# Optimization experiments

Hardware: AMD Instinct MI355X
Metric: run time of the kernel (lower is better)

The kernel has to match this reference:

```python
import jax, jax.numpy as jnp
import numpy as np

B, C, D, E, ES, TOPK = 8, 4096, 1024, 16, 256, 4096

def setup_inputs() -> dict:
    key = jax.random.key(0)
    k1, k2, k3, k4 = jax.random.split(key, 4)
    x = jax.random.normal(k1, (B, C, D), dtype=jnp.float32)
    gate = jax.random.normal(k2, (C, E), dtype=jnp.float32) / np.sqrt(D)
    lin1_weight = jax.random.normal(k3, (D, E, ES), dtype=jnp.float32) / np.sqrt(D)
    lin2_weight = jax.random.normal(k4, (E, ES, D), dtype=jnp.float32) / np.sqrt(ES)
    return {"x": x, "gate": gate, "lin1_weight": lin1_weight, "lin2_weight": lin2_weight, "topk": TOPK}

def reference(x, gate, lin1_weight, lin2_weight, topk):
    b, c, d = x.shape
    e = gate.shape[1]
    n_tokens = b * c
    # faithful to original einsum: sum x over dmodel, elementwise-mult by gate[c, e]
    gate_out = jnp.einsum('bcd,ce->bce', x, gate)            # [b, c, e]
    gate_out = jnp.transpose(gate_out, (2, 0, 1)).reshape(e, n_tokens)
    gate_out = jax.nn.softmax(gate_out, axis=1)              # softmax over tokens per expert
    topk_values, topk_indices = jax.lax.top_k(gate_out, topk)  # [e, k]
    xf = x.reshape(n_tokens, d)
    flat_idx = topk_indices.reshape(-1)
    gathered = xf[flat_idx].reshape(e, topk, d)              # dispatch
    h = jax.nn.relu(jnp.einsum('ekd,des->eks', gathered, lin1_weight))
    out = jnp.einsum('eks,esd->ekd', h, lin2_weight)
    out = out * topk_values[..., None]                       # weight by gate probs
    z = jnp.zeros_like(xf).at[flat_idx].add(out.reshape(-1, d))  # scatter-add combine
    return z.reshape(b, c, d)
```

## Files before the change

### kernel.cpp

```cpp
#include <hip/hip_runtime.h>
#include <hip/hip_bf16.h>

#define BB 8
#define CC 4096
#define DD 1024
#define EE 16
#define ESS 256
#define KSEL 4096
#define NTOK (BB*CC)
#define HLS 264

typedef short bf16x8 __attribute__((ext_vector_type(8)));
typedef float f32x4 __attribute__((ext_vector_type(4)));
typedef unsigned u32x4 __attribute__((ext_vector_type(4)));

struct PickRes { unsigned tau; unsigned n_gt; unsigned n_tie; float sm; };
struct Sel1 { unsigned b; unsigned above; unsigned kth; };

__device__ __forceinline__ short f2bf(float f) {
  unsigned u = __float_as_uint(f);
  u += 0x7FFFu + ((u >> 16) & 1u);
  return (short)(u >> 16);
}
__device__ __forceinline__ float bf2f(short s) {
  return __uint_as_float(((unsigned)(unsigned short)s) << 16);
}
__device__ __forceinline__ unsigned f2key(float f) {
  unsigned u = __float_as_uint(f);
  return (u & 0x80000000u) ? ~u : (u | 0x80000000u);
}

#define ASG __attribute__((address_space(1)))
#define ASL __attribute__((address_space(3)))
__device__ __forceinline__ void gl_lds16(void* l, const void* g) {
  __builtin_amdgcn_global_load_lds((ASG const unsigned*)g, (ASL unsigned*)l, 16, 0, 0);
}

__global__ void k_logits(const float* __restrict__ x, const float* __restrict__ gate,
                         float* __restrict__ logits, short* __restrict__ xb,
                         int* __restrict__ inv) {
  int wid = threadIdx.x >> 6, lane = threadIdx.x & 63;
  int t = blockIdx.x * 4 + wid;
  const float4* xr = reinterpret_cast<const float4*>(x + (size_t)t * DD);
  short4* xw = reinterpret_cast<short4*>(xb + (size_t)t * DD);
  float s = 0.f;
#pragma unroll
  for (int i = 0; i < 4; ++i) {
    float4 v = xr[lane + 64 * i];
    s += v.x + v.y + v.z + v.w;
    short4 p;
    p.x = f2bf(v.x); p.y = f2bf(v.y); p.z = f2bf(v.z); p.w = f2bf(v.w);
    xw[lane + 64 * i] = p;
  }
#pragma unroll
  for (int off = 32; off; off >>= 1) s += __shfl_xor(s, off);
  if (lane < EE) {
    int c = t & (CC - 1);
    logits[(size_t)lane * NTOK + t] = s * gate[c * EE + lane];
    inv[(size_t)t * EE + lane] = -1;
  }
}

__global__ __launch_bounds__(1024) void k_hist(const float* __restrict__ logits,
                                               unsigned* __restrict__ ghist,
                                               float* __restrict__ separt) {
  int e = blockIdx.x & 15, seg = blockIdx.x >> 4;
  const float* L = logits + (size_t)e * NTOK + seg * 4096;
  unsigned* Hh = ghist + (size_t)e * 65536;
  int tid = threadIdx.x;
  float sl = 0.f;
#pragma unroll
  for (int i = 0; i < 4; ++i) {
    float lv = L[tid + 1024 * i];
    atomicAdd(&Hh[f2key(lv) >> 16], 1u);
    sl += expf(lv);
  }
  __shared__ float red[1024];
  red[tid] = sl; __syncthreads();
  for (int s2 = 512; s2; s2 >>= 1) {
    if (tid < s2) red[tid] += red[tid + s2];
    __syncthreads();
  }
  if (tid == 0) separt[e * 8 + seg] = red[0];
}

__global__ __launch_bounds__(1024) void k_scan64k(
    const unsigned* __restrict__ hist, const Sel1* __restrict__ s1in, int phase,
    Sel1* __restrict__ s1out, const float* __restrict__ separt,
    PickRes* __restrict__ pres) {
  int e = blockIdx.x;
  const unsigned* Hh = hist + (size_t)e * 65536;
  int tid = threadIdx.x;
  __shared__ unsigned u0[1024], u1[1024];
  __shared__ unsigned sh_b, sh_above, sh_kth;
  unsigned target = (phase == 1) ? (unsigned)KSEL : s1in[e].kth;
  unsigned cs = 0;
  for (int j = 0; j < 64; ++j) cs += Hh[tid * 64 + j];
  u0[tid] = cs; __syncthreads();
  unsigned* src = u0; unsigned* dst = u1;
  for (int d2 = 1; d2 < 1024; d2 <<= 1) {
    unsigned v = src[tid] + ((tid + d2 < 1024) ? src[tid + d2] : 0u);
    dst[tid] = v; __syncthreads();
    unsigned* tmp = src; src = dst; dst = tmp;
  }
  unsigned above = (tid < 1023) ? src[tid + 1] : 0u;
  if (above < target && target <= src[tid]) {
    unsigned cum = above;
    for (int j = 63; j >= 0; --j) {
      unsigned h = Hh[tid * 64 + j];
      if (cum + h >= target) { sh_b = (unsigned)(tid * 64 + j); sh_above = cum; sh_kth = target - cum; break; }
      cum += h;
    }
  }
  __syncthreads();
  if (tid == 0) {
    if (phase == 1) {
      Sel1 s; s.b = sh_b; s.above = sh_above; s.kth = sh_kth;
      s1out[e] = s;
    } else {
      unsigned tau = (s1in[e].b << 16) | sh_b;
      unsigned n_gt = s1in[e].above + sh_above;
      float sm = 0.f;
      for (int j = 0; j < 8; ++j) sm += separt[e * 8 + j];
      PickRes pr; pr.tau = tau; pr.n_gt = n_gt; pr.n_tie = KSEL - n_gt; pr.sm = sm;
      pres[e] = pr;
    }
  }
}

__global__ __launch_bounds__(1024) void k_refine(const float* __restrict__ logits,
                                                 const Sel1* __restrict__ s1,
                                                 unsigned* __restrict__ hist2) {
  int e = blockIdx.x & 15, seg = blockIdx.x >> 4;
  unsigned p16 = s1[e].b;
  const float* L = logits + (size_t)e * NTOK + seg * 4096;
  unsigned* Hh = hist2 + (size_t)e * 65536;
  int tid = threadIdx.x;
#pragma unroll
  for (int i = 0; i < 4; ++i) {
    unsigned key = f2key(L[tid + 1024 * i]);
    if ((key >> 16) == p16) atomicAdd(&Hh[key & 0xFFFF], 1u);
  }
}

__global__ __launch_bounds__(1024) void k_count(const float* __restrict__ logits,
                                                const PickRes* __restrict__ pres,
                                                unsigned* __restrict__ cnts) {
  int e = blockIdx.x & 15, seg = blockIdx.x >> 4;
  PickRes pr = pres[e];
  const float* L = logits + (size_t)e * NTOK + seg * 4096;
  int tid = threadIdx.x;
  unsigned pk = 0;
#pragma unroll
  for (int i = 0; i < 4; ++i) {
    unsigned key = f2key(L[tid + 1024 * i]);
    pk += (key > pr.tau) ? 0x10000u : ((key == pr.tau) ? 1u : 0u);
  }
  __shared__ unsigned red[1024];
  red[tid] = pk; __syncthreads();
  for (int s2 = 512; s2; s2 >>= 1) {
    if (tid < s2) red[tid] += red[tid + s2];
    __syncthreads();
  }
  if (tid == 0) cnts[e * 8 + seg] = red[0];
}

__global__ void k_scan(const unsigned* __restrict__ cnts, unsigned* __restrict__ bases) {
  int e = threadIdx.x;
  if (e < EE) {
    unsigned gb = 0, qb = 0;
    for (int s = 0; s < 8; ++s) {
      unsigned c = cnts[e * 8 + s];
      bases[e * 8 + s] = (gb << 16) | qb;
      gb += c >> 16; qb += c & 0xFFFFu;
    }
  }
}

__global__ __launch_bounds__(1024) void k_compact(const float* __restrict__ logits,
                                                  const PickRes* __restrict__ pres,
                                                  const unsigned* __restrict__ bases,
                                                  int* __restrict__ sel_idx,
                                                  float* __restrict__ sel_val,
                                                  int* __restrict__ inv) {
  int e = blockIdx.x & 15, seg = blockIdx.x >> 4;
  PickRes pr = pres[e];
  const float* L = logits + (size_t)e * NTOK;
  unsigned b = bases[e * 8 + seg];
  __shared__ unsigned wtg[16], wtq[16];
  __shared__ unsigned base_g, base_q;
  int tid = threadIdx.x, wid = tid >> 6, lane = tid & 63;
  if (tid == 0) { base_g = b >> 16; base_q = b & 0xFFFFu; }
  __syncthreads();
#pragma unroll 1
  for (int i = 0; i < 4; ++i) {
    int t = seg * 4096 + tid + 1024 * i;
    float lv = L[t];
    unsigned key = f2key(lv);
    bool g = key > pr.tau, q = key == pr.tau;
    unsigned long long bg = __ballot(g), bq = __ballot(q);
    unsigned long long lm = (1ull << lane) - 1ull;
    unsigned pg = __popcll(bg & lm), pq = __popcll(bq & lm);
    if (lane == 63) { wtg[wid] = pg + (g ? 1u : 0u); wtq[wid] = pq + (q ? 1u : 0u); }
    __syncthreads();
    unsigned og = base_g, oq = base_q;
    for (int w2 = 0; w2 < wid; ++w2) { og += wtg[w2]; oq += wtq[w2]; }
    unsigned slot = 0xFFFFFFFFu;
    if (g) slot = og + pg;
    else if (q) {
      unsigned r = oq + pq;
      if (r < pr.n_tie) slot = pr.n_gt + r;
    }
    if (slot != 0xFFFFFFFFu) {
      sel_idx[(size_t)e * KSEL + slot] = t;
      sel_val[(size_t)e * KSEL + slot] = expf(lv) / pr.sm;
      inv[(size_t)t * EE + e] = e * KSEL + (int)slot;
    }
    __syncthreads();
    if (tid == 0) {
      unsigned sg = 0, sq = 0;
#pragma unroll
      for (int w2 = 0; w2 < 16; ++w2) { sg += wtg[w2]; sq += wtq[w2]; }
      base_g += sg; base_q += sq;
    }
    __syncthreads();
  }
}

__global__ void k_transpose(const float* __restrict__ src, short* __restrict__ dst,
                            int R, int C) {
  __shared__ float tile[64][65];
  int c0 = blockIdx.x * 64, r0 = blockIdx.y * 64, b = blockIdx.z;
  const float* S = src + (size_t)b * R * C;
  short* Dp = dst + (size_t)b * R * C;
  int tx = threadIdx.x & 63, ty = threadIdx.x >> 6;
#pragma unroll
  for (int i = 0; i < 16; ++i) {
    int r = ty + 4 * i;
    tile[r][tx] = S[(size_t)(r0 + r) * C + c0 + tx];
  }
  __syncthreads();
#pragma unroll
  for (int i = 0; i < 16; ++i) {
    int cR = ty + 4 * i;
    Dp[(size_t)(c0 + cR) * R + r0 + tx] = f2bf(tile[tx][cR]);
  }
}

__global__ __launch_bounds__(512, 2) void k_ff(
    const short* __restrict__ xb, const short* __restrict__ W1T,
    const short* __restrict__ W2T, const int* __restrict__ sel_idx,
    const float* __restrict__ sel_val, short* __restrict__ out) {
  int bid = blockIdx.x;
  int e = (bid & 7) + ((bid >> 9) << 3);
  int m0 = ((bid >> 3) & 63) * 64;
  __shared__ short Hl[64 * HLS];
  __shared__ bf16x8 As8[64 * 8];
  __shared__ bf16x8 Bs8[256 * 8];
  int tid = threadIdx.x, lane = tid & 63, wid = tid >> 6;
  int wr = wid >> 2, wc = wid & 3;
  const int* idxE = sel_idx + (size_t)e * KSEL;
  f32x4 acc[2][4] = {};

  int rowA = tid >> 3, sA = tid & 7;
  int xk = rowA & 7;
  const short* aSrc = xb + (size_t)idxE[m0 + rowA] * DD + (sA ^ xk) * 8;
  const short* w1Base = W1T + (size_t)e * ESS * DD + (size_t)rowA * DD + (sA ^ xk) * 8;
  const short* w2Base = W2T + (size_t)e * DD * ESS + (size_t)rowA * ESS + (sA ^ xk) * 8;

  for (int kt = 0; kt < DD / 64; ++kt) {
    int kofs = kt * 64;
    gl_lds16(&As8[tid], aSrc + kofs);
#pragma unroll
    for (int j = 0; j < 4; ++j)
      gl_lds16(&Bs8[j * 512 + tid], w1Base + (size_t)(64 * j) * DD + kofs);
    __syncthreads();
    bf16x8 af[2][2];
#pragma unroll
    for (int mg = 0; mg < 2; ++mg) {
      int row = wr * 32 + mg * 16 + (lane & 15);
#pragma unroll
      for (int h = 0; h < 2; ++h) {
        int seg = h * 4 + (lane >> 4);
        af[mg][h] = As8[row * 8 + (seg ^ (row & 7))];
      }
    }
#pragma unroll
    for (int ng = 0; ng < 4; ++ng) {
      int rowb = wc * 64 + ng * 16 + (lane & 15);
      bf16x8 b0 = Bs8[rowb * 8 + (((lane >> 4) + 0) ^ (rowb & 7))];
      bf16x8 b1 = Bs8[rowb * 8 + (((lane >> 4) + 4) ^ (rowb & 7))];
#pragma unroll
      for (int mg = 0; mg < 2; ++mg) {
        acc[mg][ng] = __builtin_amdgcn_mfma_f32_16x16x32_bf16(af[mg][0], b0, acc[mg][ng], 0, 0, 0);
        acc[mg][ng] = __builtin_amdgcn_mfma_f32_16x16x32_bf16(af[mg][1], b1, acc[mg][ng], 0, 0, 0);
      }
    }
    __syncthreads();
  }
#pragma unroll
  for (int j = 0; j < 4; ++j)
    gl_lds16(&Bs8[j * 512 + tid], w2Base + (size_t)(64 * j) * ESS);
#pragma unroll
  for (int mg = 0; mg < 2; ++mg) {
#pragma unroll
    for (int r = 0; r < 4; ++r) {
      int hrow = wr * 32 + mg * 16 + (lane >> 4) * 4 + r;
      float v = sel_val[(size_t)e * KSEL + m0 + hrow];
#pragma unroll
      for (int ng = 0; ng < 4; ++ng) {
        int col = wc * 64 + ng * 16 + (lane & 15);
        Hl[hrow * HLS + col] = f2bf(fmaxf(acc[mg][ng][r], 0.f) * v);
      }
    }
  }
  __syncthreads();
  f32x4 acc2[2][4] = {};
#pragma unroll 1
  for (int s = 0; s < 16; ++s) {
    int kt = s & 3;
    bf16x8 af[2][2];
#pragma unroll
    for (int mg = 0; mg < 2; ++mg) {
      int row = wr * 32 + mg * 16 + (lane & 15);
#pragma unroll
      for (int h = 0; h < 2; ++h) {
        int s8 = h * 4 + (lane >> 4);
        af[mg][h] = *reinterpret_cast<const bf16x8*>(&Hl[row * HLS + kt * 64 + s8 * 8]);
      }
    }
#pragma unroll
    for (int ng = 0; ng < 4; ++ng) {
      int rowb = wc * 64 + ng * 16 + (lane & 15);
      bf16x8 b0 = Bs8[rowb * 8 + (((lane >> 4) + 0) ^ (rowb & 7))];
      bf16x8 b1 = Bs8[rowb * 8 + (((lane >> 4) + 4) ^ (rowb & 7))];
#pragma unroll
      for (int mg = 0; mg < 2; ++mg) {
        acc2[mg][ng] = __builtin_amdgcn_mfma_f32_16x16x32_bf16(af[mg][0], b0, acc2[mg][ng], 0, 0, 0);
        acc2[mg][ng] = __builtin_amdgcn_mfma_f32_16x16x32_bf16(af[mg][1], b1, acc2[mg][ng], 0, 0, 0);
      }
    }
    __syncthreads();
    if (s < 15) {
      int s2 = s + 1;
      int np2 = s2 >> 2, kt2 = s2 & 3;
#pragma unroll
      for (int j = 0; j < 4; ++j)
        gl_lds16(&Bs8[j * 512 + tid],
                 w2Base + (size_t)(np2 * 256 + 64 * j) * ESS + kt2 * 64);
    }
    if (kt == 3) {
      int np = s >> 2;
      int n0 = np * 256;
#pragma unroll
      for (int mg = 0; mg < 2; ++mg) {
#pragma unroll
        for (int r = 0; r < 4; ++r) {
          int ml = wr * 32 + mg * 16 + (lane >> 4) * 4 + r;
          short* orow = out + ((size_t)(e * KSEL + m0 + ml)) * DD + n0 + wc * 64 + (lane & 15);
#pragma unroll
          for (int ng = 0; ng < 4; ++ng) orow[ng * 16] = f2bf(acc2[mg][ng][r]);
        }
      }
#pragma unroll
      for (int mg = 0; mg < 2; ++mg)
#pragma unroll
        for (int ng = 0; ng < 4; ++ng) {
          f32x4 zz = {0.f, 0.f, 0.f, 0.f};
          acc2[mg][ng] = zz;
        }
    }
    if (s < 15) __syncthreads();
  }
}

__global__ __launch_bounds__(512, 4) void k_gemm1(
    const short* __restrict__ xb, const short* __restrict__ W1T,
    const int* __restrict__ sel_idx, const float* __restrict__ sel_val,
    short* __restrict__ H) {
  int bid = blockIdx.x;
  int m0 = ((bid >> 3) & 31) * 128;
  int e = (bid & 7) + ((bid >> 8) << 3);
  __shared__ bf16x8 As8[128 * 8];
  __shared__ bf16x8 Bs8[256 * 8];
  int tid = threadIdx.x, lane = tid & 63, wid = tid >> 6;
  int wr = wid >> 2, wc = wid & 3;
  const int* idxE = sel_idx + (size_t)e * KSEL;
  f32x4 acc[4][4] = {};

  int rowA = tid >> 3, sA = tid & 7;
  int xk = rowA & 7;
  const short* aSrc0 = xb + (size_t)idxE[m0 + rowA] * DD + (sA ^ xk) * 8;
  const short* aSrc1 = xb + (size_t)idxE[m0 + rowA + 64] * DD + (sA ^ xk) * 8;
  const short* wBase = W1T + (size_t)e * ESS * DD + (size_t)rowA * DD + (sA ^ xk) * 8;

  for (int kt = 0; kt < DD / 64; ++kt) {
    int kofs = kt * 64;
    gl_lds16(&As8[tid], aSrc0 + kofs);
    gl_lds16(&As8[512 + tid], aSrc1 + kofs);
#pragma unroll
    for (int j = 0; j < 4; ++j)
      gl_lds16(&Bs8[j * 512 + tid], wBase + (size_t)(64 * j) * DD + kofs);
    __syncthreads();
    bf16x8 af[4][2];
#pragma unroll
    for (int mg = 0; mg < 4; ++mg) {
      int row = wr * 64 + mg * 16 + (lane & 15);
#pragma unroll
      for (int h = 0; h < 2; ++h) {
        int seg = h * 4 + (lane >> 4);
        af[mg][h] = As8[row * 8 + (seg ^ (row & 7))];
      }
    }
#pragma unroll
    for (int ng = 0; ng < 4; ++ng) {
      int rowb = wc * 64 + ng * 16 + (lane & 15);
      bf16x8 b0 = Bs8[rowb * 8 + (((lane >> 4) + 0) ^ (rowb & 7))];
      bf16x8 b1 = Bs8[rowb * 8 + (((lane >> 4) + 4) ^ (rowb & 7))];
#pragma unroll
      for (int mg = 0; mg < 4; ++mg) {
        acc[mg][ng] = __builtin_amdgcn_mfma_f32_16x16x32_bf16(af[mg][0], b0, acc[mg][ng], 0, 0, 0);
        acc[mg][ng] = __builtin_amdgcn_mfma_f32_16x16x32_bf16(af[mg][1], b1, acc[mg][ng], 0, 0, 0);
      }
    }
    __syncthreads();
  }
#pragma unroll
  for (int mg = 0; mg < 4; ++mg) {
#pragma unroll
    for (int r = 0; r < 4; ++r) {
      int ml = wr * 64 + mg * 16 + (lane >> 4) * 4 + r;
      float v = sel_val[(size_t)e * KSEL + m0 + ml];
      short* hrow = H + ((size_t)(e * KSEL + m0 + ml)) * ESS + wc * 64 + (lane & 15);
#pragma unroll
      for (int ng = 0; ng < 4; ++ng) {
        float o = fmaxf(acc[mg][ng][r], 0.f) * v;
        hrow[ng * 16] = f2bf(o);
      }
    }
  }
}

__global__ __launch_bounds__(512, 4) void k_gemm2_atomic(
    const short* __restrict__ H, const short* __restrict__ W2T,
    const int* __restrict__ sel_idx, float* __restrict__ z) {
  int bid = blockIdx.x;
  int p = (bid & 7) + ((bid >> 8) << 3);
  int m0 = ((bid >> 3) & 31) * 128;
  int n0 = (p & 3) * 256;
  int e = p >> 2;
  __shared__ bf16x8 As8[128 * 8];
  __shared__ bf16x8 Bs8[256 * 8];
  int tid = threadIdx.x, lane = tid & 63, wid = tid >> 6;
  int wr = wid >> 2, wc = wid & 3;
  f32x4 acc[4][4] = {};

  int rowA = tid >> 3, sA = tid & 7;
  int xk = rowA & 7;
  const short* hBase = H + (size_t)(e * KSEL + m0 + rowA) * ESS + (sA ^ xk) * 8;
  const short* w2Base = W2T + (size_t)(e * DD + n0 + rowA) * ESS + (sA ^ xk) * 8;

  for (int kt = 0; kt < ESS / 64; ++kt) {
    int kofs = kt * 64;
    gl_lds16(&As8[tid], hBase + kofs);
    gl_lds16(&As8[512 + tid], hBase + (size_t)64 * ESS + kofs);
#pragma unroll
    for (int j = 0; j < 4; ++j)
      gl_lds16(&Bs8[j * 512 + tid], w2Base + (size_t)(64 * j) * ESS + kofs);
    __syncthreads();
    bf16x8 af[4][2];
#pragma unroll
    for (int mg = 0; mg < 4; ++mg) {
      int row = wr * 64 + mg * 16 + (lane & 15);
#pragma unroll
      for (int h = 0; h < 2; ++h) {
        int seg = h * 4 + (lane >> 4);
        af[mg][h] = As8[row * 8 + (seg ^ (row & 7))];
      }
    }
#pragma unroll
    for (int ng = 0; ng < 4; ++ng) {
      int rowb = wc * 64 + ng * 16 + (lane & 15);
      bf16x8 b0 = Bs8[rowb * 8 + (((lane >> 4) + 0) ^ (rowb & 7))];
      bf16x8 b1 = Bs8[rowb * 8 + (((lane >> 4) + 4) ^ (rowb & 7))];
#pragma unroll
      for (int mg = 0; mg < 4; ++mg) {
        acc[mg][ng] = __builtin_amdgcn_mfma_f32_16x16x32_bf16(af[mg][0], b0, acc[mg][ng], 0, 0, 0);
        acc[mg][ng] = __builtin_amdgcn_mfma_f32_16x16x32_bf16(af[mg][1], b1, acc[mg][ng], 0, 0, 0);
      }
    }
    __syncthreads();
  }
#pragma unroll
  for (int mg = 0; mg < 4; ++mg) {
#pragma unroll
    for (int r = 0; r < 4; ++r) {
      int ml = wr * 64 + mg * 16 + (lane >> 4) * 4 + r;
      int token = sel_idx[(size_t)e * KSEL + m0 + ml];
      float* zr = z + (size_t)token * DD + n0 + wc * 64 + (lane & 15);
#pragma unroll
      for (int ng = 0; ng < 4; ++ng) atomicAdd(zr + ng * 16, acc[mg][ng][r]);
    }
  }
}

__global__ __launch_bounds__(256) void k_combine(const short* __restrict__ out,
                                                 const int* __restrict__ inv,
                                                 float* __restrict__ z) {
  int wid = threadIdx.x >> 6, lane = threadIdx.x & 63;
  int tA = (blockIdx.x * 4 + wid) * 2;
  int tB = tA + 1;
  int gA[16], gB[16];
  const int4* ivA = reinterpret_cast<const int4*>(inv + (size_t)tA * EE);
  const int4* ivB = reinterpret_cast<const int4*>(inv + (size_t)tB * EE);
#pragma unroll
  for (int q = 0; q < 4; ++q) {
    int4 va = ivA[q];
    gA[4 * q] = va.x; gA[4 * q + 1] = va.y; gA[4 * q + 2] = va.z; gA[4 * q + 3] = va.w;
    int4 vb = ivB[q];
    gB[4 * q] = vb.x; gB[4 * q + 1] = vb.y; gB[4 * q + 2] = vb.z; gB[4 * q + 3] = vb.w;
  }
  float accA[16] = {}, accB[16] = {};
#pragma unroll
  for (int e = 0; e < EE; ++e) {
    if (gA[e] >= 0) {
      const u32x4* rp = reinterpret_cast<const u32x4*>(out + (size_t)gA[e] * DD + lane * 16);
      u32x4 v0 = rp[0], v1 = rp[1];
      const short* s0 = reinterpret_cast<const short*>(&v0);
      const short* s1 = reinterpret_cast<const short*>(&v1);
#pragma unroll
      for (int i = 0; i < 8; ++i) { accA[i] += bf2f(s0[i]); accA[8 + i] += bf2f(s1[i]); }
    }
    if (gB[e] >= 0) {
      const u32x4* rp = reinterpret_cast<const u32x4*>(out + (size_t)gB[e] * DD + lane * 16);
      u32x4 v0 = rp[0], v1 = rp[1];
      const short* s0 = reinterpret_cast<const short*>(&v0);
      const short* s1 = reinterpret_cast<const short*>(&v1);
#pragma unroll
      for (int i = 0; i < 8; ++i) { accB[i] += bf2f(s0[i]); accB[8 + i] += bf2f(s1[i]); }
    }
  }
  float4* zwA = reinterpret_cast<float4*>(z + (size_t)tA * DD + lane * 16);
  float4* zwB = reinterpret_cast<float4*>(z + (size_t)tB * DD + lane * 16);
#pragma unroll
  for (int i = 0; i < 4; ++i) {
    float4 oa;
    oa.x = accA[4 * i]; oa.y = accA[4 * i + 1]; oa.z = accA[4 * i + 2]; oa.w = accA[4 * i + 3];
    zwA[i] = oa;
    float4 ob;
    ob.x = accB[4 * i]; ob.y = accB[4 * i + 1]; ob.z = accB[4 * i + 2]; ob.w = accB[4 * i + 3];
    zwB[i] = ob;
  }
}

extern "C" void kernel_launch(void* const* d_in, const int* in_sizes, int n_in,
                              void* d_out, int out_size, void* d_ws, size_t ws_size,
                              hipStream_t stream) {
  (void)in_sizes; (void)n_in;
  const float* x = (const float*)d_in[0];
  const float* gate = (const float*)d_in[1];
  const float* lin1 = (const float*)d_in[2];
  const float* lin2 = (const float*)d_in[3];
  float* z = (float*)d_out;

  char* ws = (char*)d_ws;
  size_t off = 0;
  auto alloc = [&](size_t bytes) -> void* {
    off = (off + 255) & ~(size_t)255;
    void* p = ws + off;
    off += bytes;
    return p;
  };
  float* logits = (float*)alloc((size_t)EE * NTOK * 4);
  int* sidx = (int*)alloc((size_t)EE * KSEL * 4);
  float* sval = (float*)alloc((size_t)EE * KSEL * 4);
  int* inv = (int*)alloc((size_t)NTOK * EE * 4);
  short* W1T = (short*)alloc((size_t)EE * ESS * DD * 2);
  short* W2T = (short*)alloc((size_t)EE * DD * ESS * 2);
  short* H = (short*)alloc((size_t)EE * KSEL * ESS * 2);
  short* xb = (short*)alloc((size_t)NTOK * DD * 2);
  size_t out_bytes = (size_t)EE * KSEL * DD * 2;
  bool combine = (off + 256 + out_bytes) <= ws_size;
  short* outbuf = combine ? (short*)alloc(out_bytes) : nullptr;

  unsigned* ghist = (unsigned*)H;
  unsigned* hist2 = (unsigned*)((char*)H + (size_t)4 * 1024 * 1024);
  float* separt = (float*)((char*)H + (size_t)8 * 1024 * 1024);
  Sel1* s1 = (Sel1*)((char*)separt + 1024);
  PickRes* pres = (PickRes*)((char*)s1 + 1024);
  unsigned* cnts = (unsigned*)((char*)pres + 1024);
  unsigned* bases = (unsigned*)((char*)cnts + 1024);

  k_transpose<<<dim3(64, 16, 1), 256, 0, stream>>>(lin1, W1T, DD, EE * ESS);
  k_transpose<<<dim3(16, 4, 16), 256, 0, stream>>>(lin2, W2T, ESS, DD);
  k_logits<<<NTOK / 4, 256, 0, stream>>>(x, gate, logits, xb, inv);
  hipMemsetAsync(ghist, 0, (size_t)8 * 1024 * 1024, stream);
  k_hist<<<128, 1024, 0, stream>>>(logits, ghist, separt);
  k_scan64k<<<EE, 1024, 0, stream>>>(ghist, s1, 1, s1, separt, pres);
  k_refine<<<128, 1024, 0, stream>>>(logits, s1, hist2);
  k_scan64k<<<EE, 1024, 0, stream>>>(hist2, s1, 2, s1, separt, pres);
  k_count<<<128, 1024, 0, stream>>>(logits, pres, cnts);
  k_scan<<<1, 64, 0, stream>>>(cnts, bases);
  k_compact<<<128, 1024, 0, stream>>>(logits, pres, bases, sidx, sval, inv);
  if (combine) {
    k_ff<<<1024, 512, 0, stream>>>(xb, W1T, W2T, sidx, sval, outbuf);
    k_combine<<<NTOK / 8, 256, 0, stream>>>(outbuf, inv, z);
  } else {
    hipMemsetAsync(d_out, 0, (size_t)out_size * sizeof(float), stream);
    k_gemm1<<<512, 512, 0, stream>>>(xb, W1T, sidx, sval, H);
    k_gemm2_atomic<<<2048, 512, 0, stream>>>(H, W2T, sidx, z);
  }
}
```

Before: 314.4 us.

## Double-buffer LDS tiles in fused FF kernel with 32-wide K steps

Restructures both GEMM phases of k_ff to use double-buffered LDS tiles. Each step works on a K slice of 32 instead of 64, and the next slice's global-to-LDS loads are issued before the MFMAs on the current buffer, so one barrier per step replaces two. The aim is to overlap memory latency with compute. In exchange it takes twice as many loop iterations with fewer MFMAs per barrier, and the LDS footprint stays about the same.

```diff
diff --git a/kernel.cpp b/kernel.cpp
--- a/kernel.cpp
+++ b/kernel.cpp
@@ -255,52 +255,58 @@
   int e = (bid & 7) + ((bid >> 9) << 3);
   int m0 = ((bid >> 3) & 63) * 64;
   __shared__ short Hl[64 * HLS];
-  __shared__ bf16x8 As8[64 * 8];
-  __shared__ bf16x8 Bs8[256 * 8];
+  __shared__ bf16x8 Ab[2][256];
+  __shared__ bf16x8 Bb[2][1024];
   int tid = threadIdx.x, lane = tid & 63, wid = tid >> 6;
   int wr = wid >> 2, wc = wid & 3;
   const int* idxE = sel_idx + (size_t)e * KSEL;
   f32x4 acc[2][4] = {};
 
-  int rowA = tid >> 3, sA = tid & 7;
-  int xk = rowA & 7;
-  const short* aSrc = xb + (size_t)idxE[m0 + rowA] * DD + (sA ^ xk) * 8;
-  const short* w1Base = W1T + (size_t)e * ESS * DD + (size_t)rowA * DD + (sA ^ xk) * 8;
-  const short* w2Base = W2T + (size_t)e * DD * ESS + (size_t)rowA * ESS + (sA ^ xk) * 8;
-
-  for (int kt = 0; kt < DD / 64; ++kt) {
-    int kofs = kt * 64;
-    gl_lds16(&As8[tid], aSrc + kofs);
-#pragma unroll
-    for (int j = 0; j < 4; ++j)
-      gl_lds16(&Bs8[j * 512 + tid], w1Base + (size_t)(64 * j) * DD + kofs);
-    __syncthreads();
-    bf16x8 af[2][2];
-#pragma unroll
-    for (int mg = 0; mg < 2; ++mg) {
-      int row = wr * 32 + mg * 16 + (lane & 15);
-#pragma unroll
-      for (int h = 0; h < 2; ++h) {
-        int seg = h * 4 + (lane >> 4);
-        af[mg][h] = As8[row * 8 + (seg ^ (row & 7))];
-      }
-    }
-#pragma unroll
-    for (int ng = 0; ng < 4; ++ng) {
-      int rowb = wc * 64 + ng * 16 + (lane & 15);
-      bf16x8 b0 = Bs8[rowb * 8 + (((lane >> 4) + 0) ^ (rowb & 7))];
-      bf16x8 b1 = Bs8[rowb * 8 + (((lane >> 4) + 4) ^ (rowb & 7))];
-#pragma unroll
-      for (int mg = 0; mg < 2; ++mg) {
-        acc[mg][ng] = __builtin_amdgcn_mfma_f32_16x16x32_bf16(af[mg][0], b0, acc[mg][ng], 0, 0, 0);
-        acc[mg][ng] = __builtin_amdgcn_mfma_f32_16x16x32_bf16(af[mg][1], b1, acc[mg][ng], 0, 0, 0);
-      }
-    }
-    __syncthreads();
-  }
-#pragma unroll
-  for (int j = 0; j < 4; ++j)
-    gl_lds16(&Bs8[j * 512 + tid], w2Base + (size_t)(64 * j) * ESS);
+  int rowA = tid >> 2, sA = tid & 3;
+  const short* aPtr = (tid < 256)
+      ? xb + (size_t)idxE[m0 + rowA] * DD + ((sA ^ (rowA & 3)) * 8) : nullptr;
+  int rowB0 = tid >> 2, sB = tid & 3;
+  int rowB1 = 128 + rowB0;
+  const short* w1e = W1T + (size_t)e * ESS * DD;
+  const short* w1p0 = w1e + (size_t)rowB0 * DD + ((sB ^ (rowB0 & 3)) * 8);
+  const short* w1p1 = w1e + (size_t)rowB1 * DD + ((sB ^ (rowB1 & 3)) * 8);
+  const short* w2e = W2T + (size_t)e * DD * ESS;
+  const short* w2p0 = w2e + (size_t)rowB0 * ESS + ((sB ^ (rowB0 & 3)) * 8);
+  const short* w2p1 = w2e + (size_t)rowB1 * ESS + ((sB ^ (rowB1 & 3)) * 8);
+
+  {
+    if (tid < 256) gl_lds16(&Ab[0][tid], aPtr);
+    gl_lds16(&Bb[0][tid], w1p0);
+    gl_lds16(&Bb[0][512 + tid], w1p1);
+    __syncthreads();
+#pragma unroll 1
+    for (int ks = 0; ks < 32; ++ks) {
+      int cur = ks & 1;
+      if (ks < 31) {
+        int ko = (ks + 1) * 32;
+        if (tid < 256) gl_lds16(&Ab[cur ^ 1][tid], aPtr + ko);
+        gl_lds16(&Bb[cur ^ 1][tid], w1p0 + ko);
+        gl_lds16(&Bb[cur ^ 1][512 + tid], w1p1 + ko);
+      }
+      bf16x8 a0, a1;
+      {
+        int r0 = wr * 32 + (lane & 15);
+        a0 = Ab[cur][r0 * 4 + ((lane >> 4) ^ (r0 & 3))];
+        int r1 = r0 + 16;
+        a1 = Ab[cur][r1 * 4 + ((lane >> 4) ^ (r1 & 3))];
+      }
+#pragma unroll
+      for (int ng = 0; ng < 4; ++ng) {
+        int rb = wc * 64 + ng * 16 + (lane & 15);
+        bf16x8 b = Bb[cur][rb * 4 + ((lane >> 4) ^ (rb & 3))];
+        acc[0][ng] = __builtin_amdgcn_mfma_f32_16x16x32_bf16(a0, b, acc[0][ng], 0, 0, 0);
+        acc[1][ng] = __builtin_amdgcn_mfma_f32_16x16x32_bf16(a1, b, acc[1][ng], 0, 0, 0);
+      }
+      __syncthreads();
+    }
+  }
+  gl_lds16(&Bb[0][tid], w2p0);
+  gl_lds16(&Bb[0][512 + tid], w2p1);
 #pragma unroll
   for (int mg = 0; mg < 2; ++mg) {
 #pragma unroll
@@ -317,41 +323,31 @@
   __syncthreads();
   f32x4 acc2[2][4] = {};
 #pragma unroll 1
-  for (int s = 0; s < 16; ++s) {
-    int kt = s & 3;
-    bf16x8 af[2][2];
-#pragma unroll
-    for (int mg = 0; mg < 2; ++mg) {
-      int row = wr * 32 + mg * 16 + (lane & 15);
-#pragma unroll
-      for (int h = 0; h < 2; ++h) {
-        int s8 = h * 4 + (lane >> 4);
-        af[mg][h] = *reinterpret_cast<const bf16x8*>(&Hl[row * HLS + kt * 64 + s8 * 8]);
-      }
+  for (int s = 0; s < 32; ++s) {
+    int cur = s & 1;
+    if (s < 31) {
+      int s2 = s + 1;
+      size_t off2 = (size_t)((s2 >> 3) * 256) * ESS + (s2 & 7) * 32;
+      gl_lds16(&Bb[cur ^ 1][tid], w2p0 + off2);
+      gl_lds16(&Bb[cur ^ 1][512 + tid], w2p1 + off2);
+    }
+    int ksub = s & 7;
+    bf16x8 a0, a1;
+    {
+      int r0 = wr * 32 + (lane & 15);
+      a0 = *reinterpret_cast<const bf16x8*>(&Hl[r0 * HLS + ksub * 32 + (lane >> 4) * 8]);
+      int r1 = r0 + 16;
+      a1 = *reinterpret_cast<const bf16x8*>(&Hl[r1 * HLS + ksub * 32 + (lane >> 4) * 8]);
     }
 #pragma unroll
     for (int ng = 0; ng < 4; ++ng) {
-      int rowb = wc * 64 + ng * 16 + (lane & 15);
-      bf16x8 b0 = Bs8[rowb * 8 + (((lane >> 4) + 0) ^ (rowb & 7))];
-      bf16x8 b1 = Bs8[rowb * 8 + (((lane >> 4) + 4) ^ (rowb & 7))];
-#pragma unroll
-      for (int mg = 0; mg < 2; ++mg) {
-        acc2[mg][ng] = __builtin_amdgcn_mfma_f32_16x16x32_bf16(af[mg][0], b0, acc2[mg][ng], 0, 0, 0);
-        acc2[mg][ng] = __builtin_amdgcn_mfma_f32_16x16x32_bf16(af[mg][1], b1, acc2[mg][ng], 0, 0, 0);
-      }
-    }
-    __syncthreads();
-    if (s < 15) {
-      int s2 = s + 1;
-      int np2 = s2 >> 2, kt2 = s2 & 3;
-#pragma unroll
-      for (int j = 0; j < 4; ++j)
-        gl_lds16(&Bs8[j * 512 + tid],
-                 w2Base + (size_t)(np2 * 256 + 64 * j) * ESS + kt2 * 64);
-    }
-    if (kt == 3) {
-      int np = s >> 2;
-      int n0 = np * 256;
+      int rb = wc * 64 + ng * 16 + (lane & 15);
+      bf16x8 b = Bb[cur][rb * 4 + ((lane >> 4) ^ (rb & 3))];
+      acc2[0][ng] = __builtin_amdgcn_mfma_f32_16x16x32_bf16(a0, b, acc2[0][ng], 0, 0, 0);
+      acc2[1][ng] = __builtin_amdgcn_mfma_f32_16x16x32_bf16(a1, b, acc2[1][ng], 0, 0, 0);
+    }
+    if (ksub == 7) {
+      int n0 = (s >> 3) * 256;
 #pragma unroll
       for (int mg = 0; mg < 2; ++mg) {
 #pragma unroll
@@ -370,7 +366,7 @@
           acc2[mg][ng] = zz;
         }
     }
-    if (s < 15) __syncthreads();
+    __syncthreads();
   }
 }
 
```

Measured after the change: 325.7 us. 3.6% more time.
